# Performance work log

Hardware: AMD Instinct MI355X
Metric: run time of the kernel (lower is better)

## Reference

```python
import jax, jax.numpy as jnp
import numpy as np

B, V, C = 2, 6, 96
D, H, W = 48, 48, 48
TH, TW = 96, 96
EPS = 1e-5


def _trilinear_sample_zeros(vol, gx, gy, gz):
    # vol: [B,C,D,H,W]; gx/gy/gz: normalized coords [D,H,W]; align_corners=False, zeros padding
    Dd, Hh, Ww = vol.shape[2], vol.shape[3], vol.shape[4]
    ix = ((gx + 1.0) * Ww - 1.0) * 0.5
    iy = ((gy + 1.0) * Hh - 1.0) * 0.5
    iz = ((gz + 1.0) * Dd - 1.0) * 0.5
    x0 = jnp.floor(ix); y0 = jnp.floor(iy); z0 = jnp.floor(iz)
    tx, ty, tz = ix - x0, iy - y0, iz - z0
    out = jnp.zeros(vol.shape, vol.dtype)
    for dz in (0, 1):
        for dy in (0, 1):
            for dx in (0, 1):
                xc, yc, zc = x0 + dx, y0 + dy, z0 + dz
                w = ((tx if dx else 1.0 - tx) * (ty if dy else 1.0 - ty)
                     * (tz if dz else 1.0 - tz))
                inb = ((xc >= 0) & (xc < Ww) & (yc >= 0) & (yc < Hh)
                       & (zc >= 0) & (zc < Dd))
                xi = jnp.clip(xc, 0, Ww - 1).astype(jnp.int32)
                yi = jnp.clip(yc, 0, Hh - 1).astype(jnp.int32)
                zi = jnp.clip(zc, 0, Dd - 1).astype(jnp.int32)
                val = vol[:, :, zi, yi, xi]  # [B,C,D,H,W]
                out = out + val * (w * inb)[None, None]
    return out


def _resize_bilinear(img, oh, ow):
    # torch F.interpolate(mode='bilinear', align_corners=False) semantics
    h, w = img.shape[-2], img.shape[-1]
    def idx(n_in, n_out):
        scale = n_in / n_out
        src = jnp.maximum(scale * (jnp.arange(n_out) + 0.5) - 0.5, 0.0)
        i0 = jnp.clip(jnp.floor(src).astype(jnp.int32), 0, n_in - 1)
        i1 = jnp.clip(i0 + 1, 0, n_in - 1)
        return i0, i1, (src - i0).astype(img.dtype)
    y0, y1, ty = idx(h, oh)
    x0, x1, tx = idx(w, ow)
    rows = img[..., y0, :] * (1.0 - ty)[:, None] + img[..., y1, :] * ty[:, None]
    return rows[..., x0] * (1.0 - tx) + rows[..., x1] * tx


def _project_one_view(vol, theta):
    # base grid per torch affine_grid(align_corners=False): pixel-center coords in [-1,1]
    zc = (jnp.arange(D) + 0.5) * (2.0 / D) - 1.0
    yc = (jnp.arange(H) + 0.5) * (2.0 / H) - 1.0
    xc = (jnp.arange(W) + 0.5) * (2.0 / W) - 1.0
    Z, Y, X = jnp.meshgrid(zc, yc, xc, indexing='ij')  # [D,H,W]
    c, s = jnp.cos(theta), jnp.sin(theta)
    gx = c * X + s * Z   # rotation about Y axis, rows [c,0,s],[0,1,0],[-s,0,c]
    gy = Y
    gz = -s * X + c * Z
    rotated = _trilinear_sample_zeros(vol, gx, gy, gz)  # [B,C,D,H,W]
    feat2d = rotated.mean(axis=2)                       # depth mean -> [B,C,H,W]
    return _resize_bilinear(feat2d, TH, TW)             # [B,C,TH,TW]


def _post(x, conv1_w, bn_gamma, bn_beta, conv2_w, conv2_b):
    dn = ('NCHW', 'OIHW', 'NCHW')
    x = jax.lax.conv_general_dilated(x, conv1_w, (1, 1), 'SAME', dimension_numbers=dn)
    mu = x.mean(axis=(0, 2, 3), keepdims=True)
    var = ((x - mu) ** 2).mean(axis=(0, 2, 3), keepdims=True)  # biased var, train-mode BN
    x = (x - mu) * jax.lax.rsqrt(var + EPS)
    x = x * bn_gamma[None, :, None, None] + bn_beta[None, :, None, None]
    x = jax.nn.gelu(x, approximate=False)
    x = jax.lax.conv_general_dilated(x, conv2_w, (1, 1), 'SAME', dimension_numbers=dn)
    return x + conv2_b[None, :, None, None]


def setup_inputs() -> dict:
    key = jax.random.key(0)
    k0, k1, k2 = jax.random.split(key, 3)
    voxel_tokens = jax.random.normal(k0, (B, D * H * W, C), jnp.float32)
    view_angles = jnp.linspace(0.0, 2.0 * np.pi, V + 1)[:-1].astype(jnp.float32)
    conv1_w = jax.random.normal(k1, (C, C, 3, 3), jnp.float32) / np.sqrt(C * 9.0)
    bn_gamma = jnp.ones((C,), jnp.float32)
    bn_beta = jnp.zeros((C,), jnp.float32)
    conv2_w = jax.random.normal(k2, (C, C, 1, 1), jnp.float32) / np.sqrt(C)
    conv2_b = jnp.zeros((C,), jnp.float32)
    return dict(voxel_tokens=voxel_tokens, view_angles=view_angles,
                conv1_w=conv1_w, bn_gamma=bn_gamma, bn_beta=bn_beta,
                conv2_w=conv2_w, conv2_b=conv2_b)


def reference(voxel_tokens, view_angles, conv1_w, bn_gamma, bn_beta, conv2_w, conv2_b):
    b = voxel_tokens.shape[0]
    vol = voxel_tokens.transpose(0, 2, 1).reshape(b, C, D, H, W)
    feats = jax.vmap(lambda th: _project_one_view(vol, th))(view_angles)  # [V,B,C,TH,TW]
    # BN stats are computed per-view (torch applies self.post inside the view loop)
    posted = jax.vmap(lambda f: _post(f, conv1_w, bn_gamma, bn_beta, conv2_w, conv2_b))(feats)
    return posted.transpose(1, 0, 2, 3, 4)  # [B,V,C,TH,TW]
```

## Files before the change

### kernel.cpp

```cpp
#include <hip/hip_runtime.h>
#include <math.h>

#define Bn 2
#define Vn 6
#define Cn 96
#define Dn 48
#define Hn 48
#define Wn 48
#define THn 96
#define TWn 96
#define EPSf 1e-5f

#define PD 98
#define NCI8 12
#define RZ_VB (PD * NCI8 * PD * 8)
#define RZ_BYTES (12 * RZ_VB * 2)

typedef __attribute__((ext_vector_type(8))) short s8v;
typedef __attribute__((ext_vector_type(4))) float f4v;

__device__ __forceinline__ unsigned short f2bf(float f) {
    unsigned int u = __builtin_bit_cast(unsigned int, f);
    u += 0x7FFFu + ((u >> 16) & 1u);
    return (unsigned short)(u >> 16);
}
__device__ __forceinline__ float bf2f(unsigned short h) {
    unsigned int u = ((unsigned int)h) << 16;
    return __builtin_bit_cast(float, u);
}
__device__ __forceinline__ void unpack8(uint4 r, float* f) {
    unsigned int w[4] = {r.x, r.y, r.z, r.w};
#pragma unroll
    for (int j = 0; j < 8; ++j)
        f[j] = bf2f((unsigned short)((w[j >> 1] >> ((j & 1) * 16)) & 0xFFFFu));
}
__device__ __forceinline__ uint4 pack8(const unsigned short* o) {
    uint4 pk;
    pk.x = (unsigned int)o[0] | ((unsigned int)o[1] << 16);
    pk.y = (unsigned int)o[2] | ((unsigned int)o[3] << 16);
    pk.z = (unsigned int)o[4] | ((unsigned int)o[5] << 16);
    pk.w = (unsigned int)o[6] | ((unsigned int)o[7] << 16);
    return pk;
}

__device__ __forceinline__ float gelu_f(float y) {
    float z = y * 0.70710678118654752f;
    float a = fabsf(z);
    float t = __builtin_amdgcn_rcpf(fmaf(0.3275911f, a, 1.0f));
    float e = __builtin_amdgcn_exp2f(-1.4426950408889634f * a * a);
    float p = t * fmaf(t, fmaf(t, fmaf(t, fmaf(t, 1.061405429f,
                                               -1.453152027f),
                                       1.421413741f),
                               -0.284496736f),
                       0.254829592f);
    float er = fmaf(-p, e, 1.0f);
    er = copysignf(er, z);
    return 0.5f * y * (1.0f + er);
}

__global__ __launch_bounds__(256) void k_prep(const float* __restrict__ w1,
                                              const float* __restrict__ w2,
                                              unsigned short* __restrict__ wAtP,
                                              unsigned short* __restrict__ wCP) {
    int i = blockIdx.x * 256 + threadIdx.x;
    if (i < 82944) {
        int e = i & 7;
        int u = i >> 3;
        int co = u % 96;
        int u2 = u / 96;
        int ci8 = u2 % NCI8;
        int tap = u2 / NCI8;
        wAtP[i] = f2bf(w1[(co * 96 + ci8 * 8 + e) * 9 + tap]);
    } else if (i < 92160) {
        int j = i - 82944;
        int e = j & 7;
        int u = j >> 3;
        int co = u % 96;
        int ci8 = u / 96;
        wCP[j] = f2bf(w2[co * 96 + ci8 * 8 + e]);
    }
}

__global__ __launch_bounds__(256) void k_tok(const float* __restrict__ tokens,
                                             unsigned short* __restrict__ tokB) {
    int idx = blockIdx.x * 256 + threadIdx.x;
    size_t base = (size_t)idx * 8;
    float4 f0 = *(const float4*)(tokens + base);
    float4 f1 = *(const float4*)(tokens + base + 4);
    unsigned short o[8] = {f2bf(f0.x), f2bf(f0.y), f2bf(f0.z), f2bf(f0.w),
                           f2bf(f1.x), f2bf(f1.y), f2bf(f1.z), f2bf(f1.w)};
    *(uint4*)(&tokB[base]) = pack8(o);
}

__global__ __launch_bounds__(256) void k_feat(const unsigned short* __restrict__ tokB,
                                              const float* __restrict__ angles,
                                              unsigned short* __restrict__ featP) {
    int idx = blockIdx.x * 256 + threadIdx.x;
    int c8i = idx % NCI8;
    int r = idx / NCI8;
    int x = r % Wn; r /= Wn;
    int y = r % Hn; r /= Hn;
    int b = r & 1;
    int v = r >> 1;
    int vb = v * 2 + b;

    float th = angles[v];
    float ct = cosf(th), st = sinf(th);
    float X = (x + 0.5f) * (2.0f / 48.0f) - 1.0f;
    float Zc0 = 0.5f * (2.0f / 48.0f) - 1.0f;
    float ix = 24.0f * (ct * X + st * Zc0) + 23.5f;
    float iz = 24.0f * (-st * X + ct * Zc0) + 23.5f;

    const unsigned short* tb = tokB + (size_t)b * (Dn * Hn * Wn) * Cn + c8i * 8;
    int ybase = y * Wn;

    float af[8] = {0.f, 0.f, 0.f, 0.f, 0.f, 0.f, 0.f, 0.f};
    for (int z = 0; z < Dn; ++z) {
        float x0f = floorf(ix), z0f = floorf(iz);
        float tx = ix - x0f, tz = iz - z0f;
        int x0 = (int)x0f, z0 = (int)z0f;
        float wx[2] = {1.0f - tx, tx};
        float wz[2] = {1.0f - tz, tz};
#pragma unroll
        for (int dz = 0; dz < 2; ++dz) {
            int zc = z0 + dz;
            bool zin = (zc >= 0) && (zc < Dn);
            int zi = min(max(zc, 0), Dn - 1);
            int zoff = zi * (Hn * Wn);
#pragma unroll
            for (int dx = 0; dx < 2; ++dx) {
                int xc = x0 + dx;
                bool xin = (xc >= 0) && (xc < Wn);
                int xi = min(max(xc, 0), Wn - 1);
                float w = wx[dx] * wz[dz] * ((zin && xin) ? 1.0f : 0.0f);
                uint4 raw = *(const uint4*)(tb + (size_t)(zoff + ybase + xi) * Cn);
                float f[8];
                unpack8(raw, f);
#pragma unroll
                for (int j = 0; j < 8; ++j) af[j] += w * f[j];
            }
        }
        ix += st;
        iz += ct;
    }
    const float s = 1.0f / 48.0f;
    unsigned short o[8];
#pragma unroll
    for (int j = 0; j < 8; ++j) o[j] = f2bf(af[j] * s);
    size_t off = (((size_t)vb * Hn + y) * NCI8 + c8i) * Wn + x;
    *(uint4*)(&featP[off * 8]) = pack8(o);
}

__global__ __launch_bounds__(256) void k_resize(const unsigned short* __restrict__ featP,
                                                unsigned short* __restrict__ rz) {
    int idx = blockIdx.x * 256 + threadIdx.x;
    int x = idx % TWn;
    int r = idx / TWn;
    int c8i = r % NCI8; r /= NCI8;
    int y = r % THn;
    int vb = r / THn;

    float sy = fmaxf(0.5f * (y + 0.5f) - 0.5f, 0.0f);
    int y0 = min((int)sy, Hn - 1);
    int y1 = min(y0 + 1, Hn - 1);
    float ty = sy - (float)y0;
    float sx = fmaxf(0.5f * (x + 0.5f) - 0.5f, 0.0f);
    int x0 = min((int)sx, Wn - 1);
    int x1 = min(x0 + 1, Wn - 1);
    float tx = sx - (float)x0;

    const unsigned short* fb = featP + ((size_t)vb * Hn * NCI8 + c8i) * Wn * 8;
    const unsigned short* r0 = fb + (size_t)y0 * (NCI8 * Wn * 8);
    const unsigned short* r1 = fb + (size_t)y1 * (NCI8 * Wn * 8);
    uint4 q00 = *(const uint4*)(r0 + (size_t)x0 * 8);
    uint4 q01 = *(const uint4*)(r0 + (size_t)x1 * 8);
    uint4 q10 = *(const uint4*)(r1 + (size_t)x0 * 8);
    uint4 q11 = *(const uint4*)(r1 + (size_t)x1 * 8);
    float f00[8], f01[8], f10[8], f11[8];
    unpack8(q00, f00); unpack8(q01, f01); unpack8(q10, f10); unpack8(q11, f11);

    float w00 = (1.f - ty) * (1.f - tx), w01 = (1.f - ty) * tx;
    float w10 = ty * (1.f - tx),         w11 = ty * tx;

    unsigned short o[8];
#pragma unroll
    for (int j = 0; j < 8; ++j)
        o[j] = f2bf(w00 * f00[j] + w01 * f01[j] + w10 * f10[j] + w11 * f11[j]);

    size_t off = (((size_t)vb * PD + (y + 1)) * NCI8 + c8i) * PD + (x + 1);
    *(uint4*)(&rz[off * 8]) = pack8(o);
}

__global__ __launch_bounds__(256) void k_conv1(const unsigned short* __restrict__ rz,
                                               const unsigned short* __restrict__ wAtP,
                                               unsigned short* __restrict__ co1) {
    int blk = blockIdx.x;
    int n0 = blk * 128;
    int vb = n0 / 9216;
    int nl0 = n0 - vb * 9216;

    int t = threadIdx.x;
    int wv = t >> 6;
    int l = t & 63;
    int l15 = l & 15, q = l >> 4;

    int nt0 = nl0 + wv * 32;
    int nl[2];
    const unsigned short* pB[2];
#pragma unroll
    for (int i = 0; i < 2; ++i) {
        nl[i] = nt0 + i * 16 + l15;
        int y = nl[i] / 96, x = nl[i] - y * 96;
        pB[i] = rz + ((((size_t)vb * PD + y) * NCI8) * PD + x) * 8;
    }

    f4v acc[2][6];
#pragma unroll
    for (int i = 0; i < 2; ++i)
#pragma unroll
        for (int mt = 0; mt < 6; ++mt) acc[i][mt] = (f4v){0.f, 0.f, 0.f, 0.f};

#pragma unroll
    for (int ks = 0; ks < 3; ++ks) {
        int ci8 = ks * 4 + q;
        const unsigned short* pb0 = pB[0] + (size_t)ci8 * (PD * 8);
        const unsigned short* pb1 = pB[1] + (size_t)ci8 * (PD * 8);
        const unsigned short* pa = wAtP + ((size_t)ci8 * 96 + l15) * 8;
#pragma unroll
        for (int tap = 0; tap < 9; ++tap) {
            int dy = tap / 3, dx = tap % 3;
            size_t toff = ((size_t)dy * (NCI8 * PD) + dx) * 8;
            s8v b0 = *(const s8v*)(pb0 + toff);
            s8v b1 = *(const s8v*)(pb1 + toff);
            const unsigned short* ap = pa + (size_t)tap * (NCI8 * 96 * 8);
#pragma unroll
            for (int mt = 0; mt < 6; ++mt) {
                s8v a = *(const s8v*)(ap + (size_t)mt * (16 * 8));
                acc[0][mt] = __builtin_amdgcn_mfma_f32_16x16x32_bf16(a, b0, acc[0][mt], 0, 0, 0);
                acc[1][mt] = __builtin_amdgcn_mfma_f32_16x16x32_bf16(a, b1, acc[1][mt], 0, 0, 0);
            }
        }
    }

#pragma unroll
    for (int i = 0; i < 2; ++i) {
#pragma unroll
        for (int mt = 0; mt < 6; ++mt) {
            int co0 = mt * 16 + q * 4;
            ushort4 pk;
            pk.x = f2bf(acc[i][mt][0]); pk.y = f2bf(acc[i][mt][1]);
            pk.z = f2bf(acc[i][mt][2]); pk.w = f2bf(acc[i][mt][3]);
            size_t off = (((size_t)vb * NCI8 + (co0 >> 3)) * 9216 + nl[i]) * 8 + (co0 & 7);
            *(ushort4*)(&co1[off]) = pk;
        }
    }
}

__global__ __launch_bounds__(256) void k_stats1(const unsigned short* __restrict__ co1,
                                                float* __restrict__ part) {
    int g = blockIdx.x >> 4;
    int chunk = blockIdx.x & 15;
    int v = g / NCI8;
    int c8 = g % NCI8;
    int t = threadIdx.x;

    float s[8] = {0,0,0,0,0,0,0,0}, ss[8] = {0,0,0,0,0,0,0,0};
    int m0 = chunk * 1152;
    for (int m = m0 + t; m < m0 + 1152; m += 256) {
        int bb = m / 9216;
        int n = m - bb * 9216;
        const unsigned short* p = co1 + (((size_t)(v * 2 + bb) * NCI8 + c8) * 9216 + n) * 8;
        uint4 raw = *(const uint4*)p;
        float f[8];
        unpack8(raw, f);
#pragma unroll
        for (int j = 0; j < 8; ++j) { s[j] += f[j]; ss[j] += f[j] * f[j]; }
    }
#pragma unroll
    for (int off = 1; off < 64; off <<= 1) {
#pragma unroll
        for (int j = 0; j < 8; ++j) {
            s[j]  += __shfl_xor(s[j],  off);
            ss[j] += __shfl_xor(ss[j], off);
        }
    }
    __shared__ float rs[4][8], rss[4][8];
    int wv = t >> 6;
    if ((t & 63) == 0) {
#pragma unroll
        for (int j = 0; j < 8; ++j) { rs[wv][j] = s[j]; rss[wv][j] = ss[j]; }
    }
    __syncthreads();
    if (t < 8) {
        int j = t;
        part[(size_t)blockIdx.x * 16 + j]     = rs[0][j] + rs[1][j] + rs[2][j] + rs[3][j];
        part[(size_t)blockIdx.x * 16 + 8 + j] = rss[0][j] + rss[1][j] + rss[2][j] + rss[3][j];
    }
}

__global__ __launch_bounds__(64) void k_stats2(const float* __restrict__ part,
                                               const float* __restrict__ gamma,
                                               const float* __restrict__ beta,
                                               float* __restrict__ scale,
                                               float* __restrict__ shift) {
    int g = blockIdx.x;
    int t = threadIdx.x;
    int j = t & 7, c = t >> 3;
    size_t b0 = ((size_t)g * 16 + c) * 16;
    size_t b1 = ((size_t)g * 16 + c + 8) * 16;
    float S  = part[b0 + j]     + part[b1 + j];
    float SS = part[b0 + 8 + j] + part[b1 + 8 + j];
#pragma unroll
    for (int off = 8; off < 64; off <<= 1) {
        S  += __shfl_xor(S,  off);
        SS += __shfl_xor(SS, off);
    }
    if (t < 8) {
        int v = g / NCI8, c8 = g % NCI8;
        const float invN = 1.0f / (float)(Bn * THn * TWn);
        float mu = S * invN;
        float var = SS * invN - mu * mu;
        float rstd = rsqrtf(fmaxf(var, 0.0f) + EPSf);
        int ch = c8 * 8 + j;
        float sc = rstd * gamma[ch];
        scale[v * 96 + ch] = sc;
        shift[v * 96 + ch] = beta[ch] - mu * sc;
    }
}

__global__ __launch_bounds__(256) void k_conv2(const unsigned short* __restrict__ co1,
                                               const unsigned short* __restrict__ wCP,
                                               const float* __restrict__ scale,
                                               const float* __restrict__ shift,
                                               const float* __restrict__ b2,
                                               float* __restrict__ out) {
    __shared__ float ssc[96], ssh[96], sbias[96];

    int blk = blockIdx.x;
    int n0 = blk * 64;
    int vb = n0 / 9216;
    int nl0 = n0 - vb * 9216;
    int v = vb >> 1, b = vb & 1;

    int t = threadIdx.x;
    int wv = t >> 6;
    int l = t & 63;
    int l15 = l & 15, q = l >> 4;

    if (t < 96) {
        ssc[t] = scale[v * 96 + t];
        ssh[t] = shift[v * 96 + t];
        sbias[t] = b2[t];
    }
    __syncthreads();

    int n = nl0 + wv * 16 + l15;

    f4v acc[6];
#pragma unroll
    for (int mt = 0; mt < 6; ++mt) acc[mt] = (f4v){0.f, 0.f, 0.f, 0.f};

#pragma unroll
    for (int ks = 0; ks < 3; ++ks) {
        int ci8 = ks * 4 + q;
        int ci0 = ci8 * 8;
        float sc[8], sh[8];
#pragma unroll
        for (int j = 0; j < 8; ++j) { sc[j] = ssc[ci0 + j]; sh[j] = ssh[ci0 + j]; }

        const unsigned short* pb = co1 + (((size_t)vb * NCI8 + ci8) * 9216 + n) * 8;
        uint4 raw = *(const uint4*)pb;
        float f[8];
        unpack8(raw, f);
        unsigned short o[8];
#pragma unroll
        for (int j = 0; j < 8; ++j) {
            float yv = f[j] * sc[j] + sh[j];
            o[j] = f2bf(gelu_f(yv));
        }
        s8v bfr = __builtin_bit_cast(s8v, pack8(o));

        const unsigned short* pa = wCP + ((size_t)ci8 * 96 + l15) * 8;
#pragma unroll
        for (int mt = 0; mt < 6; ++mt) {
            s8v a = *(const s8v*)(pa + (size_t)mt * (16 * 8));
            acc[mt] = __builtin_amdgcn_mfma_f32_16x16x32_bf16(a, bfr, acc[mt], 0, 0, 0);
        }
    }

    size_t obase = ((size_t)(b * Vn + v) * Cn) * 9216;
#pragma unroll
    for (int mt = 0; mt < 6; ++mt) {
        int co0 = mt * 16 + q * 4;
#pragma unroll
        for (int reg = 0; reg < 4; ++reg) {
            int co = co0 + reg;
            out[obase + (size_t)co * 9216 + n] = acc[mt][reg] + sbias[co];
        }
    }
}

extern "C" void kernel_launch(void* const* d_in, const int* in_sizes, int n_in,
                              void* d_out, int out_size, void* d_ws, size_t ws_size,
                              hipStream_t stream) {
    const float* tokens = (const float*)d_in[0];
    const float* angles = (const float*)d_in[1];
    const float* w1     = (const float*)d_in[2];
    const float* gamma  = (const float*)d_in[3];
    const float* beta   = (const float*)d_in[4];
    const float* w2     = (const float*)d_in[5];
    const float* b2     = (const float*)d_in[6];
    float* out = (float*)d_out;

    char* ws = (char*)d_ws;
    unsigned short* featP = (unsigned short*)(ws);
    float* part = (float*)(ws);
    unsigned short* tokB  = (unsigned short*)(ws + 5308416);
    unsigned short* rz    = (unsigned short*)(ws + 5308416);
    unsigned short* co1   = (unsigned short*)(ws + 27436032);
    unsigned short* wAtP  = (unsigned short*)(ws + 48669696);
    unsigned short* wCP   = (unsigned short*)(ws + 48835584);
    float* scale = (float*)(ws + 48854016);
    float* shift = (float*)(ws + 48856320);

    k_prep<<<360, 256, 0, stream>>>(w1, w2, wAtP, wCP);
    k_tok<<<10368, 256, 0, stream>>>(tokens, tokB);
    k_feat<<<1296, 256, 0, stream>>>(tokB, angles, featP);
    hipMemsetAsync(rz, 0, RZ_BYTES, stream);
    k_resize<<<5184, 256, 0, stream>>>(featP, rz);
    k_conv1<<<864, 256, 0, stream>>>(rz, wAtP, co1);
    k_stats1<<<1152, 256, 0, stream>>>(co1, part);
    k_stats2<<<72, 64, 0, stream>>>(part, gamma, beta, scale, shift);
    k_conv2<<<1728, 256, 0, stream>>>(co1, wCP, scale, shift, b2, out);
}
```

Baseline: 292.0 us.

## Precompute projection sample tables, split z-loop across lanes, zero only padding border

Merges the token-to-bf16 conversion, weight prep and a new per-view sampling-table build (bilinear weights and byte offsets per x,z) into one launch. The projection kernel now reads these tables and no longer recomputes floor, clamp and weights on every step. Each output's 48-step z loop is split across two lanes and combined with a shuffle, doubling the thread count. The full-buffer memset of the padded resize output is replaced by extra blocks in the resize kernel that zero only the border pixels. The trade-off is extra table traffic and some added indexing logic.

```diff
diff --git a/kernel.cpp b/kernel.cpp
--- a/kernel.cpp
+++ b/kernel.cpp
@@ -13,8 +13,6 @@
 
 #define PD 98
 #define NCI8 12
-#define RZ_VB (PD * NCI8 * PD * 8)
-#define RZ_BYTES (12 * RZ_VB * 2)
 
 typedef __attribute__((ext_vector_type(8))) short s8v;
 typedef __attribute__((ext_vector_type(4))) float f4v;
@@ -58,101 +56,150 @@
     return 0.5f * y * (1.0f + er);
 }
 
-__global__ __launch_bounds__(256) void k_prep(const float* __restrict__ w1,
-                                              const float* __restrict__ w2,
-                                              unsigned short* __restrict__ wAtP,
-                                              unsigned short* __restrict__ wCP) {
-    int i = blockIdx.x * 256 + threadIdx.x;
-    if (i < 82944) {
-        int e = i & 7;
-        int u = i >> 3;
-        int co = u % 96;
-        int u2 = u / 96;
-        int ci8 = u2 % NCI8;
-        int tap = u2 / NCI8;
-        wAtP[i] = f2bf(w1[(co * 96 + ci8 * 8 + e) * 9 + tap]);
-    } else if (i < 92160) {
-        int j = i - 82944;
-        int e = j & 7;
-        int u = j >> 3;
-        int co = u % 96;
-        int ci8 = u / 96;
-        wCP[j] = f2bf(w2[co * 96 + ci8 * 8 + e]);
-    }
-}
-
-__global__ __launch_bounds__(256) void k_tok(const float* __restrict__ tokens,
-                                             unsigned short* __restrict__ tokB) {
+__global__ __launch_bounds__(256) void k_pre(const float* __restrict__ tokens,
+                                             unsigned short* __restrict__ tokB,
+                                             const float* __restrict__ w1,
+                                             const float* __restrict__ w2,
+                                             unsigned short* __restrict__ wAtP,
+                                             unsigned short* __restrict__ wCP,
+                                             const float* __restrict__ angles,
+                                             float4* __restrict__ wtabW,
+                                             int4* __restrict__ wtabO) {
+    if (blockIdx.x < 10368) {
+        int idx = blockIdx.x * 256 + threadIdx.x;
+        size_t base = (size_t)idx * 8;
+        float4 f0 = *(const float4*)(tokens + base);
+        float4 f1 = *(const float4*)(tokens + base + 4);
+        unsigned short o[8] = {f2bf(f0.x), f2bf(f0.y), f2bf(f0.z), f2bf(f0.w),
+                               f2bf(f1.x), f2bf(f1.y), f2bf(f1.z), f2bf(f1.w)};
+        *(uint4*)(&tokB[base]) = pack8(o);
+    } else if (blockIdx.x < 10728) {
+        int i = (blockIdx.x - 10368) * 256 + threadIdx.x;
+        if (i < 82944) {
+            int e = i & 7;
+            int u = i >> 3;
+            int co = u % 96;
+            int u2 = u / 96;
+            int ci8 = u2 % NCI8;
+            int tap = u2 / NCI8;
+            wAtP[i] = f2bf(w1[(co * 96 + ci8 * 8 + e) * 9 + tap]);
+        } else if (i < 92160) {
+            int j = i - 82944;
+            int e = j & 7;
+            int u = j >> 3;
+            int co = u % 96;
+            int ci8 = u / 96;
+            wCP[j] = f2bf(w2[co * 96 + ci8 * 8 + e]);
+        }
+    } else {
+        int e = (blockIdx.x - 10728) * 256 + threadIdx.x;
+        if (e >= 13824) return;
+        int z = e % 48;
+        int r = e / 48;
+        int x = r % 48;
+        int v = r / 48;
+
+        float th = angles[v];
+        float ct = cosf(th), st = sinf(th);
+        float xr = (float)x + 0.5f - 24.0f;
+        float zr = (float)z + 0.5f - 24.0f;
+        float ix = ct * xr + st * zr + 23.5f;
+        float iz = -st * xr + ct * zr + 23.5f;
+
+        float x0f = floorf(ix), z0f = floorf(iz);
+        float tx = ix - x0f, tz = iz - z0f;
+        int x0 = (int)x0f, z0 = (int)z0f;
+        float wx[2] = {1.0f - tx, tx};
+        float wz[2] = {1.0f - tz, tz};
+
+        float w[4];
+        int o[4];
+#pragma unroll
+        for (int dz = 0; dz < 2; ++dz) {
+            int zc = z0 + dz;
+            bool zin = (zc >= 0) && (zc < Dn);
+            int zi = min(max(zc, 0), Dn - 1);
+#pragma unroll
+            for (int dx = 0; dx < 2; ++dx) {
+                int xc = x0 + dx;
+                bool xin = (xc >= 0) && (xc < Wn);
+                int xi = min(max(xc, 0), Wn - 1);
+                int k = dz * 2 + dx;
+                w[k] = wx[dx] * wz[dz] * ((zin && xin) ? 1.0f : 0.0f) * (1.0f / 48.0f);
+                o[k] = (zi * 221184 + xi * 96) * 2;
+            }
+        }
+        wtabW[e] = (float4){w[0], w[1], w[2], w[3]};
+        wtabO[e] = (int4){o[0], o[1], o[2], o[3]};
+    }
+}
+
+__global__ __launch_bounds__(256) void k_feat3(const unsigned short* __restrict__ tokB,
+                                               const float4* __restrict__ wtabW,
+                                               const int4* __restrict__ wtabO,
+                                               unsigned short* __restrict__ featP) {
     int idx = blockIdx.x * 256 + threadIdx.x;
-    size_t base = (size_t)idx * 8;
-    float4 f0 = *(const float4*)(tokens + base);
-    float4 f1 = *(const float4*)(tokens + base + 4);
-    unsigned short o[8] = {f2bf(f0.x), f2bf(f0.y), f2bf(f0.z), f2bf(f0.w),
-                           f2bf(f1.x), f2bf(f1.y), f2bf(f1.z), f2bf(f1.w)};
-    *(uint4*)(&tokB[base]) = pack8(o);
-}
-
-__global__ __launch_bounds__(256) void k_feat(const unsigned short* __restrict__ tokB,
-                                              const float* __restrict__ angles,
-                                              unsigned short* __restrict__ featP) {
-    int idx = blockIdx.x * 256 + threadIdx.x;
-    int c8i = idx % NCI8;
-    int r = idx / NCI8;
+    int h = idx & 1;
+    int r = idx >> 1;
+    int c8 = r % NCI8; r /= NCI8;
     int x = r % Wn; r /= Wn;
     int y = r % Hn; r /= Hn;
     int b = r & 1;
     int v = r >> 1;
     int vb = v * 2 + b;
 
-    float th = angles[v];
-    float ct = cosf(th), st = sinf(th);
-    float X = (x + 0.5f) * (2.0f / 48.0f) - 1.0f;
-    float Zc0 = 0.5f * (2.0f / 48.0f) - 1.0f;
-    float ix = 24.0f * (ct * X + st * Zc0) + 23.5f;
-    float iz = 24.0f * (-st * X + ct * Zc0) + 23.5f;
-
-    const unsigned short* tb = tokB + (size_t)b * (Dn * Hn * Wn) * Cn + c8i * 8;
-    int ybase = y * Wn;
+    int tb0 = (v * 48 + x) * 48 + h * 24;
+    const float4* tw = wtabW + tb0;
+    const int4* to = wtabO + tb0;
+    const char* tb = (const char*)tokB +
+                     ((size_t)b * 10616832 + (size_t)y * 4608 + c8 * 8) * 2;
 
     float af[8] = {0.f, 0.f, 0.f, 0.f, 0.f, 0.f, 0.f, 0.f};
-    for (int z = 0; z < Dn; ++z) {
-        float x0f = floorf(ix), z0f = floorf(iz);
-        float tx = ix - x0f, tz = iz - z0f;
-        int x0 = (int)x0f, z0 = (int)z0f;
-        float wx[2] = {1.0f - tx, tx};
-        float wz[2] = {1.0f - tz, tz};
-#pragma unroll
-        for (int dz = 0; dz < 2; ++dz) {
-            int zc = z0 + dz;
-            bool zin = (zc >= 0) && (zc < Dn);
-            int zi = min(max(zc, 0), Dn - 1);
-            int zoff = zi * (Hn * Wn);
-#pragma unroll
-            for (int dx = 0; dx < 2; ++dx) {
-                int xc = x0 + dx;
-                bool xin = (xc >= 0) && (xc < Wn);
-                int xi = min(max(xc, 0), Wn - 1);
-                float w = wx[dx] * wz[dz] * ((zin && xin) ? 1.0f : 0.0f);
-                uint4 raw = *(const uint4*)(tb + (size_t)(zoff + ybase + xi) * Cn);
-                float f[8];
-                unpack8(raw, f);
-#pragma unroll
-                for (int j = 0; j < 8; ++j) af[j] += w * f[j];
-            }
-        }
-        ix += st;
-        iz += ct;
-    }
-    const float s = 1.0f / 48.0f;
-    unsigned short o[8];
-#pragma unroll
-    for (int j = 0; j < 8; ++j) o[j] = f2bf(af[j] * s);
-    size_t off = (((size_t)vb * Hn + y) * NCI8 + c8i) * Wn + x;
-    *(uint4*)(&featP[off * 8]) = pack8(o);
+#pragma unroll 4
+    for (int k = 0; k < 24; ++k) {
+        float4 w = tw[k];
+        int4 o = to[k];
+        uint4 r0 = *(const uint4*)(tb + o.x);
+        uint4 r1 = *(const uint4*)(tb + o.y);
+        uint4 r2 = *(const uint4*)(tb + o.z);
+        uint4 r3 = *(const uint4*)(tb + o.w);
+        float f0[8], f1[8], f2[8], f3[8];
+        unpack8(r0, f0); unpack8(r1, f1); unpack8(r2, f2); unpack8(r3, f3);
+#pragma unroll
+        for (int j = 0; j < 8; ++j) {
+            af[j] += w.x * f0[j] + w.y * f1[j];
+            af[j] += w.z * f2[j] + w.w * f3[j];
+        }
+    }
+#pragma unroll
+    for (int j = 0; j < 8; ++j) af[j] += __shfl_xor(af[j], 1);
+
+    if (h == 0) {
+        unsigned short o[8];
+#pragma unroll
+        for (int j = 0; j < 8; ++j) o[j] = f2bf(af[j]);
+        size_t off = (((size_t)vb * Hn + y) * NCI8 + c8) * Wn + x;
+        *(uint4*)(&featP[off * 8]) = pack8(o);
+    }
 }
 
 __global__ __launch_bounds__(256) void k_resize(const unsigned short* __restrict__ featP,
                                                 unsigned short* __restrict__ rz) {
+    if (blockIdx.x >= 5184) {
+        int hid = (blockIdx.x - 5184) * 256 + threadIdx.x;
+        if (hid >= 55872) return;
+        int p = hid % 388;
+        int r2 = hid / 388;
+        int c8 = r2 % NCI8;
+        int vb = r2 / NCI8;
+        int py, px;
+        if (p < 98)      { py = 0;  px = p; }
+        else if (p < 196){ py = 97; px = p - 98; }
+        else { int q = p - 196; py = 1 + (q >> 1); px = (q & 1) ? 97 : 0; }
+        size_t off = (((size_t)vb * PD + py) * NCI8 + c8) * PD + px;
+        *(uint4*)(&rz[off * 8]) = (uint4){0u, 0u, 0u, 0u};
+        return;
+    }
     int idx = blockIdx.x * 256 + threadIdx.x;
     int x = idx % TWn;
     int r = idx / TWn;
@@ -414,20 +461,21 @@
 
     char* ws = (char*)d_ws;
     unsigned short* featP = (unsigned short*)(ws);
-    float* part = (float*)(ws);
+    float* part           = (float*)(ws);
     unsigned short* tokB  = (unsigned short*)(ws + 5308416);
     unsigned short* rz    = (unsigned short*)(ws + 5308416);
     unsigned short* co1   = (unsigned short*)(ws + 27436032);
+    float4* wtabW         = (float4*)(ws + 47775744);
+    int4*  wtabO          = (int4*)(ws + 47996928);
     unsigned short* wAtP  = (unsigned short*)(ws + 48669696);
     unsigned short* wCP   = (unsigned short*)(ws + 48835584);
     float* scale = (float*)(ws + 48854016);
     float* shift = (float*)(ws + 48856320);
 
-    k_prep<<<360, 256, 0, stream>>>(w1, w2, wAtP, wCP);
-    k_tok<<<10368, 256, 0, stream>>>(tokens, tokB);
-    k_feat<<<1296, 256, 0, stream>>>(tokB, angles, featP);
-    hipMemsetAsync(rz, 0, RZ_BYTES, stream);
-    k_resize<<<5184, 256, 0, stream>>>(featP, rz);
+    k_pre<<<10782, 256, 0, stream>>>(tokens, tokB, w1, w2, wAtP, wCP,
+                                     angles, wtabW, wtabO);
+    k_feat3<<<2592, 256, 0, stream>>>(tokB, wtabW, wtabO, featP);
+    k_resize<<<5403, 256, 0, stream>>>(featP, rz);
     k_conv1<<<864, 256, 0, stream>>>(rz, wAtP, co1);
     k_stats1<<<1152, 256, 0, stream>>>(co1, part);
     k_stats2<<<72, 64, 0, stream>>>(part, gamma, beta, scale, shift);
```

After: 306.5 us. 1.05x slower.
